# Performance work log

Measured on AMD Instinct MI355X. Metric: run time of the kernel, lower is better.

The kernel has to match this reference:

```python
import jax, jax.numpy as jnp
import numpy as np

N_HEADS = 32
N_KV_HEADS = 8
HEAD_DIM = 128
N_QUERY = N_HEADS // N_KV_HEADS  # 4
ROPE_BASE = 10000.0


def _rope_tables(seq_len, head_dim):
    # inv freqs over pairs of channels (Llama-style interleaved complex rotation)
    inv_freq = 1.0 / (ROPE_BASE ** (jnp.arange(0, head_dim, 2, dtype=jnp.float32) / head_dim))
    t = jnp.arange(seq_len, dtype=jnp.float32)
    ang = t[:, None] * inv_freq[None, :]           # [s, d/2]
    return jnp.cos(ang)[None, :, None, :], jnp.sin(ang)[None, :, None, :]  # [1,s,1,d/2]


def _apply_rope(x, cos, sin):
    # x: [b, s, h, d]; consecutive channel pairs are (real, imag)
    xr = x[..., 0::2]
    xi = x[..., 1::2]
    out_r = xr * cos - xi * sin
    out_i = xr * sin + xi * cos
    return jnp.stack([out_r, out_i], axis=-1).reshape(x.shape)


def setup_inputs() -> dict:
    key = jax.random.key(0)
    kx, kq, kk, kv, ko = jax.random.split(key, 5)
    dim = 4096
    kv_dim = N_KV_HEADS * HEAD_DIM
    scale = 0.02
    return {
        "x": jax.random.normal(kx, (2, 2048, dim), dtype=jnp.float32),
        "wq": jax.random.normal(kq, (dim, dim), dtype=jnp.float32) * scale,
        "wk": jax.random.normal(kk, (dim, kv_dim), dtype=jnp.float32) * scale,
        "wv": jax.random.normal(kv, (dim, kv_dim), dtype=jnp.float32) * scale,
        "wo": jax.random.normal(ko, (dim, dim), dtype=jnp.float32) * scale,
    }


def reference(x, wq, wk, wv, wo):
    b, s, _ = x.shape
    xq = (x @ wq).reshape(b, s, N_HEADS, HEAD_DIM)
    xk = (x @ wk).reshape(b, s, N_KV_HEADS, HEAD_DIM)
    xv = (x @ wv).reshape(b, s, N_KV_HEADS, HEAD_DIM)

    cos, sin = _rope_tables(s, HEAD_DIM)
    xq = _apply_rope(xq, cos, sin)
    xk = _apply_rope(xk, cos, sin)

    # GQA without materializing the KV expand: group query heads per kv head.
    qh = xq.reshape(b, s, N_KV_HEADS, N_QUERY, HEAD_DIM)
    scores = jnp.einsum('bsgnd,btgd->bgnst', qh, xk) / jnp.sqrt(
        jnp.asarray(HEAD_DIM, dtype=xq.dtype))  # [b,g,n,s,t]

    # causal mask: -inf above diagonal
    causal = jnp.arange(s)[:, None] >= jnp.arange(s)[None, :]
    scores = jnp.where(causal[None, None, None, :, :], scores, -jnp.inf)

    att = jax.nn.softmax(scores.astype(jnp.float32), axis=-1).astype(xq.dtype)
    out = jnp.einsum('bgnst,btgd->bsgnd', att, xv).reshape(b, s, N_HEADS * HEAD_DIM)
    return out @ wo
```

## Files before the change

### kernel.cpp

```cpp
#include <hip/hip_runtime.h>
#include <hip/hip_bf16.h>

typedef __attribute__((ext_vector_type(8))) short short8;
typedef __attribute__((ext_vector_type(4))) float f32x4;
typedef __attribute__((ext_vector_type(16))) float f32x16;

#define GLD16(gp, lp) __builtin_amdgcn_global_load_lds( \
    (const __attribute__((address_space(1))) unsigned int*)(gp), \
    (__attribute__((address_space(3))) unsigned int*)(lp), 16, 0, 0)

static __device__ __forceinline__ float bf2f(unsigned short u) {
    union { unsigned int i; float f; } v; v.i = ((unsigned int)u) << 16; return v.f;
}
static __device__ __forceinline__ short f2bf(float f) {
    union { float f; unsigned int i; } v; v.f = f;
    unsigned int r = v.i + 0x7FFFu + ((v.i >> 16) & 1u);
    return (short)(r >> 16);
}
static __device__ __forceinline__ unsigned int pack2bf(float lo, float hi) {
    return ((unsigned int)(unsigned short)f2bf(hi) << 16) | (unsigned int)(unsigned short)f2bf(lo);
}
static __device__ __forceinline__ unsigned int cvtpk(float lo, float hi) {
    unsigned int w;
    asm("v_cvt_pk_bf16_f32 %0, %1, %2" : "=v"(w) : "v"(lo), "v"(hi));
    return w;
}

__global__ void cast_f32_bf16(const float* __restrict__ src, short* __restrict__ dst, int n) {
    int i = (blockIdx.x * 256 + threadIdx.x) * 4;
    if (i >= n) return;
    float4 v = *(const float4*)(src + i);
    short4 o;
    o.x = f2bf(v.x); o.y = f2bf(v.y); o.z = f2bf(v.z); o.w = f2bf(v.w);
    *(short4*)(dst + i) = o;
}

__global__ void transpose_cast(const float* __restrict__ src, short* __restrict__ dst,
                               int N, int dstStride) {
    __shared__ float tile[32][33];
    int k0 = blockIdx.x * 32, n0 = blockIdx.y * 32;
    int t = threadIdx.x, c = t & 31, r = t >> 5;
#pragma unroll
    for (int p = 0; p < 4; ++p)
        tile[r + p * 8][c] = src[(size_t)(k0 + r + p * 8) * N + n0 + c];
    __syncthreads();
#pragma unroll
    for (int p = 0; p < 4; ++p)
        dst[(size_t)(n0 + r + p * 8) * dstStride + k0 + c] = f2bf(tile[c][r + p * 8]);
}

__global__ void transpose_v(const short* __restrict__ qkv, short* __restrict__ vt) {
    __shared__ short tile[32][33];
    int s0 = blockIdx.x * 32, d0 = blockIdx.y * 32;
    int bh = blockIdx.z;
    int b = bh >> 3, h = bh & 7;
    const short* src = qkv + (size_t)b * 2048 * 6144 + 5120 + h * 128;
    short* dst = vt + (size_t)bh * 128 * 2048;
    int t = threadIdx.x, c = t & 31, r = t >> 5;
#pragma unroll
    for (int p = 0; p < 4; ++p)
        tile[r + p * 8][c] = src[(size_t)(s0 + r + p * 8) * 6144 + d0 + c];
    __syncthreads();
#pragma unroll
    for (int p = 0; p < 4; ++p)
        dst[(size_t)(d0 + r + p * 8) * 2048 + s0 + c] = tile[c][r + p * 8];
}

__global__ void rope_tables(float* __restrict__ cs) {
    int i = blockIdx.x * 256 + threadIdx.x;
    int s = i >> 6, d2 = i & 63;
    float inv = expf(-9.210340371976184f * (float)(2 * d2) * (1.0f / 128.0f));
    float ang = (float)s * inv;
    float sn, c;
    sincosf(ang, &sn, &c);
    cs[(size_t)i * 2] = c;
    cs[(size_t)i * 2 + 1] = sn;
}

template<int NH>
__global__ void rope_apply(const short* __restrict__ qkv, const float* __restrict__ cs,
                           short* __restrict__ dst, int colOff, float scale) {
    int i = blockIdx.x * 256 + threadIdx.x;
    int d2 = i & 63;
    int t2 = i >> 6;
    int h = t2 % NH;
    int bs = t2 / NH;
    int s = bs & 2047;
    int b = bs >> 11;
    unsigned int pr = *(const unsigned int*)(qkv + (size_t)bs * 6144 + colOff + h * 128 + 2 * d2);
    float xr = bf2f((unsigned short)(pr & 0xFFFFu));
    float xi = bf2f((unsigned short)(pr >> 16));
    const float* cp = cs + ((size_t)s * 64 + d2) * 2;
    float c = cp[0], sn = cp[1];
    float outr = (xr * c - xi * sn) * scale;
    float outi = (xr * sn + xi * c) * scale;
    *(unsigned int*)(dst + ((size_t)(b * NH + h) * 2048 + s) * 128 + 2 * d2) = pack2bf(outr, outi);
}

template<bool BF16OUT>
__global__ __launch_bounds__(512, 1) void gemm256(const short* __restrict__ A,
                                                  const short* __restrict__ Bt,
                                                  void* __restrict__ Cv,
                                                  int Mtiles, int N, int K) {
    extern __shared__ __align__(16) short lds[];
    short* As = lds;
    short* Bs = lds + 32768;
    const int tid = threadIdx.x;
    const int lane = tid & 63;
    const int wid = tid >> 6;
    const int lr = lane & 15;
    const int lq = lane >> 4;
    const int wr = wid >> 2;
    const int wc = wid & 3;

    const int nwg = gridDim.x;
    const int id = blockIdx.x;
    const int sid = (id & 7) * (nwg >> 3) + (id >> 3);
    const int m0 = (sid % Mtiles) * 256;
    const int n0 = (sid / Mtiles) * 256;

    const short* aBase = A + (size_t)m0 * K;
    const short* bBase = Bt + (size_t)n0 * K;
    const int NT = K >> 5;

    auto stage = [&](int t) {
        const int buf = t & 3;
#pragma unroll
        for (int j = 0; j < 2; ++j) {
            int cl = j * 512 + tid;
            int lrw = cl >> 3;
            int cs = (cl & 7) ^ (lrw & 7);
            int trow = lrw + ((cs & 4) << 5);
            int kc = (cs & 3) * 8;
            GLD16(aBase + (size_t)trow * K + t * 32 + kc, As + buf * 8192 + cl * 8);
        }
#pragma unroll
        for (int j = 0; j < 2; ++j) {
            int cl = j * 512 + tid;
            int lrw = cl >> 3;
            int cs = (cl & 7) ^ (lrw & 7);
            int trow = lrw + ((cs & 4) << 5);
            int kc = (cs & 3) * 8;
            GLD16(bBase + (size_t)trow * K + t * 32 + kc, Bs + buf * 8192 + cl * 8);
        }
    };

    f32x4 acc[8][4];
#pragma unroll
    for (int mi = 0; mi < 8; ++mi)
#pragma unroll
        for (int ni = 0; ni < 4; ++ni) acc[mi][ni] = f32x4{0.f, 0.f, 0.f, 0.f};

    stage(0); stage(1); stage(2);
    asm volatile("s_waitcnt vmcnt(8)" ::: "memory");
    __builtin_amdgcn_sched_barrier(0);
    __builtin_amdgcn_s_barrier();
    __builtin_amdgcn_sched_barrier(0);

    for (int t = 0; t < NT; ++t) {
        const int buf = t & 3;
        if (t + 3 < NT) stage(t + 3);

        short8 af[8], bfr[4];
#pragma unroll
        for (int mi = 0; mi < 8; ++mi) {
            int lrw = (wr * 128 + mi * 16 + lr) & 127;
            int chunk = ((wr << 2) | lq) ^ (lrw & 7);
            af[mi] = *(const short8*)(As + buf * 8192 + lrw * 64 + chunk * 8);
        }
#pragma unroll
        for (int ni = 0; ni < 4; ++ni) {
            int tc = wc * 64 + ni * 16 + lr;
            int lrw = tc & 127;
            int chunk = (((tc >> 7) << 2) | lq) ^ (lrw & 7);
            bfr[ni] = *(const short8*)(Bs + buf * 8192 + lrw * 64 + chunk * 8);
        }

        __builtin_amdgcn_s_setprio(1);
#pragma unroll
        for (int mi = 0; mi < 8; ++mi)
#pragma unroll
            for (int ni = 0; ni < 4; ++ni)
                acc[mi][ni] = __builtin_amdgcn_mfma_f32_16x16x32_bf16(af[mi], bfr[ni], acc[mi][ni], 0, 0, 0);
        __builtin_amdgcn_s_setprio(0);

        __builtin_amdgcn_sched_barrier(0);
        if (t + 3 < NT)       { asm volatile("s_waitcnt vmcnt(8)" ::: "memory"); }
        else if (t + 3 == NT) { asm volatile("s_waitcnt vmcnt(4)" ::: "memory"); }
        else if (t + 2 == NT) { asm volatile("s_waitcnt vmcnt(0)" ::: "memory"); }
        __builtin_amdgcn_sched_barrier(0);
        if (t + 1 < NT) {
            __builtin_amdgcn_s_barrier();
            __builtin_amdgcn_sched_barrier(0);
        }
    }

#pragma unroll
    for (int mi = 0; mi < 8; ++mi)
#pragma unroll
        for (int ni = 0; ni < 4; ++ni)
#pragma unroll
            for (int r = 0; r < 4; ++r) {
                int row = m0 + wr * 128 + mi * 16 + lq * 4 + r;
                int col = n0 + wc * 64 + ni * 16 + lr;
                float v = acc[mi][ni][r];
                if constexpr (BF16OUT) ((short*)Cv)[(size_t)row * N + col] = f2bf(v);
                else                   ((float*)Cv)[(size_t)row * N + col] = v;
            }
}

__global__ __launch_bounds__(256, 2) void attn_kernel(const short* __restrict__ Qr,
                                                      const short* __restrict__ Kr,
                                                      const short* __restrict__ Vt,
                                                      short* __restrict__ Out) {
    __shared__ short Ks[64 * 128];
    __shared__ short Vs[128 * 64];
    const int qb = 15 - blockIdx.x;
    const int bh = blockIdx.y;
    const int b = bh >> 5;
    const int qh = bh & 31;
    const int kvh = qh >> 2;
    const int tid = threadIdx.x;
    const int lane = tid & 63;
    const int w = tid >> 6;
    const int l31 = lane & 31;
    const int hi = lane >> 5;
    const int qg0 = qb * 128 + w * 32;

    const short* qbase = Qr + ((size_t)bh * 2048 + qg0 + l31) * 128 + hi * 8;
    short8 qf[8];
#pragma unroll
    for (int ks = 0; ks < 8; ++ks)
        qf[ks] = *(const short8*)(qbase + ks * 16);

    const short* kbase = Kr + (size_t)(b * 8 + kvh) * 2048 * 128;
    const short* vbase = Vt + (size_t)(b * 8 + kvh) * 128 * 2048;

    float m_run = -INFINITY, l_run = 0.0f;
    f32x16 oacc[4];
#pragma unroll
    for (int dt = 0; dt < 4; ++dt) oacc[dt] = f32x16{0,0,0,0,0,0,0,0,0,0,0,0,0,0,0,0};

    const int nkb = 2 * qb + 2;
    for (int kb = 0; kb < nkb; ++kb) {
        const int s0 = kb * 64;
#pragma unroll
        for (int j = 0; j < 4; ++j) {
            int c = j * 256 + tid;
            int krow = c >> 4;
            int kcol = ((c & 15) ^ (krow & 7)) * 8;
            GLD16(kbase + (size_t)(s0 + krow) * 128 + kcol, Ks + (size_t)c * 8);
            int vrow = c >> 3;
            int vcol = ((c & 7) ^ (vrow & 7)) * 8;
            GLD16(vbase + (size_t)vrow * 2048 + s0 + vcol, Vs + (size_t)c * 8);
        }
        __syncthreads();

        if (s0 <= qg0 + 31) {
            f32x16 st0 = f32x16{0,0,0,0,0,0,0,0,0,0,0,0,0,0,0,0};
            f32x16 st1 = f32x16{0,0,0,0,0,0,0,0,0,0,0,0,0,0,0,0};
            __builtin_amdgcn_s_setprio(1);
#pragma unroll
            for (int ks = 0; ks < 8; ++ks) {
                int row0 = l31;
                int ch0 = ((2 * ks + hi) ^ (row0 & 7)) * 8;
                short8 kf0 = *(const short8*)(Ks + row0 * 128 + ch0);
                st0 = __builtin_amdgcn_mfma_f32_32x32x16_bf16(kf0, qf[ks], st0, 0, 0, 0);
                int row1 = 32 + l31;
                int ch1 = ((2 * ks + hi) ^ (row1 & 7)) * 8;
                short8 kf1 = *(const short8*)(Ks + row1 * 128 + ch1);
                st1 = __builtin_amdgcn_mfma_f32_32x32x16_bf16(kf1, qf[ks], st1, 0, 0, 0);
            }
            __builtin_amdgcn_s_setprio(0);

            const int q = qg0 + l31;
            if (s0 + 63 > qg0) {
#pragma unroll
                for (int i = 0; i < 16; ++i) {
                    int kvr = (i & 3) + 8 * (i >> 2) + 4 * hi;
                    if (s0 + kvr > q)      st0[i] = -INFINITY;
                    if (s0 + 32 + kvr > q) st1[i] = -INFINITY;
                }
            }

            float mx = -INFINITY;
#pragma unroll
            for (int i = 0; i < 16; ++i) mx = fmaxf(mx, fmaxf(st0[i], st1[i]));
            mx = fmaxf(mx, __shfl_xor(mx, 32, 64));

            const bool defer = __all(mx - m_run <= 8.0f);
            float mN, alpha;
            if (defer) { mN = m_run; alpha = 1.0f; }
            else       { mN = fmaxf(m_run, mx); alpha = __expf(m_run - mN); }

            float p0[16], p1[16];
            float rsum = 0.0f;
#pragma unroll
            for (int i = 0; i < 16; ++i) {
                p0[i] = __expf(st0[i] - mN);
                p1[i] = __expf(st1[i] - mN);
                rsum += p0[i] + p1[i];
            }
            rsum += __shfl_xor(rsum, 32, 64);
            l_run = l_run * alpha + rsum;
            m_run = mN;
            if (!defer) {
#pragma unroll
                for (int dt = 0; dt < 4; ++dt)
#pragma unroll
                    for (int i = 0; i < 16; ++i) oacc[dt][i] *= alpha;
            }

            short8 pfr[4];
#pragma unroll
            for (int kvs = 0; kvs < 4; ++kvs) {
                const float* pp = (kvs < 2) ? p0 : p1;
                const int h8 = (kvs & 1) * 8;
                unsigned int x0 = cvtpk(pp[h8 + 0], pp[h8 + 1]);
                unsigned int x1 = cvtpk(pp[h8 + 2], pp[h8 + 3]);
                unsigned int y0 = cvtpk(pp[h8 + 4], pp[h8 + 5]);
                unsigned int y1 = cvtpk(pp[h8 + 6], pp[h8 + 7]);
                asm("v_permlane32_swap_b32 %0, %1" : "+v"(x0), "+v"(y0));
                asm("v_permlane32_swap_b32 %0, %1" : "+v"(x1), "+v"(y1));
                union { unsigned int u[4]; short8 s; } uu;
                uu.u[0] = x0; uu.u[1] = x1; uu.u[2] = y0; uu.u[3] = y1;
                pfr[kvs] = uu.s;
            }

            __builtin_amdgcn_s_setprio(1);
#pragma unroll
            for (int dt = 0; dt < 4; ++dt) {
                int row = dt * 32 + l31;
#pragma unroll
                for (int kvs = 0; kvs < 4; ++kvs) {
                    int ch = ((2 * kvs + hi) ^ (row & 7)) * 8;
                    short8 vf = *(const short8*)(Vs + row * 64 + ch);
                    oacc[dt] = __builtin_amdgcn_mfma_f32_32x32x16_bf16(vf, pfr[kvs], oacc[dt], 0, 0, 0);
                }
            }
            __builtin_amdgcn_s_setprio(0);
        }
        __syncthreads();
    }

    const float inv = 1.0f / l_run;
    const size_t row = (size_t)b * 2048 + qg0 + l31;
    short* obase = Out + row * 4096 + qh * 128;
#pragma unroll
    for (int dt = 0; dt < 4; ++dt) {
#pragma unroll
        for (int g = 0; g < 4; ++g) {
            short4 o4;
            o4.x = f2bf(oacc[dt][g * 4 + 0] * inv);
            o4.y = f2bf(oacc[dt][g * 4 + 1] * inv);
            o4.z = f2bf(oacc[dt][g * 4 + 2] * inv);
            o4.w = f2bf(oacc[dt][g * 4 + 3] * inv);
            *(short4*)(obase + dt * 32 + g * 8 + hi * 4) = o4;
        }
    }
}


extern "C" void kernel_launch(void* const* d_in, const int* in_sizes, int n_in,
                              void* d_out, int out_size, void* d_ws, size_t ws_size,
                              hipStream_t stream) {
    const float* x  = (const float*)d_in[0];
    const float* wq = (const float*)d_in[1];
    const float* wk = (const float*)d_in[2];
    const float* wv = (const float*)d_in[3];
    const float* wo = (const float*)d_in[4];
    float* out = (float*)d_out;
    char* ws = (char*)d_ws;

    short* wt_qkv = (short*)(ws + 0);
    short* xb     = (short*)(ws + 50331648);
    short* qkv    = (short*)(ws + 83886080);
    short* wt_o   = (short*)(ws + 83886080);
    short* qr     = (short*)(ws + 134217728);
    short* kr     = (short*)(ws + 167772160);
    short* vt     = (short*)(ws + 176160768);
    float* tab    = (float*)(ws + 184549376);

    cast_f32_bf16<<<16384, 256, 0, stream>>>(x, xb, 16777216);
    transpose_cast<<<dim3(128, 128), 256, 0, stream>>>(wq, wt_qkv, 4096, 4096);
    transpose_cast<<<dim3(128, 32),  256, 0, stream>>>(wk, wt_qkv + (size_t)4096 * 4096, 1024, 4096);
    transpose_cast<<<dim3(128, 32),  256, 0, stream>>>(wv, wt_qkv + (size_t)5120 * 4096, 1024, 4096);
    rope_tables<<<512, 256, 0, stream>>>(tab);
    gemm256<true><<<384, 512, 131072, stream>>>(xb, wt_qkv, (void*)qkv, 16, 6144, 4096);
    rope_apply<32><<<32768, 256, 0, stream>>>(qkv, tab, qr, 0, 0.08838834764831845f);
    rope_apply<8><<<8192, 256, 0, stream>>>(qkv, tab, kr, 4096, 1.0f);
    transpose_v<<<dim3(64, 4, 16), 256, 0, stream>>>(qkv, vt);
    transpose_cast<<<dim3(128, 128), 256, 0, stream>>>(wo, wt_o, 4096, 4096);
    attn_kernel<<<dim3(16, 64), 256, 0, stream>>>(qr, kr, vt, xb);
    gemm256<false><<<256, 512, 131072, stream>>>(xb, wt_o, (void*)out, 16, 4096, 4096);
}
```

Measured before the change: 617.9 us.

## Split GEMM K-step into two MFMA phases with interleaved A/B staging

The bf16 GEMM main loop now runs each K-step in two halves. Each half reads its four A fragments from LDS, issues one operand's global-to-LDS prefetch (A in the first half, B in the second), and then runs a 4x4 block of MFMAs. The aim is to interleave LDS reads, global prefetches and matrix math more finely so memory latency hides behind compute. The cost is extra workgroup barriers and lgkmcnt waits per iteration, which may add sync stalls.

```diff
diff --git a/kernel.cpp b/kernel.cpp
--- a/kernel.cpp
+++ b/kernel.cpp
@@ -123,7 +123,7 @@
     const short* bBase = Bt + (size_t)n0 * K;
     const int NT = K >> 5;
 
-    auto stage = [&](int t) {
+    auto stageA = [&](int t) {
         const int buf = t & 3;
 #pragma unroll
         for (int j = 0; j < 2; ++j) {
@@ -134,6 +134,9 @@
             int kc = (cs & 3) * 8;
             GLD16(aBase + (size_t)trow * K + t * 32 + kc, As + buf * 8192 + cl * 8);
         }
+    };
+    auto stageB = [&](int t) {
+        const int buf = t & 3;
 #pragma unroll
         for (int j = 0; j < 2; ++j) {
             int cl = j * 512 + tid;
@@ -151,7 +154,7 @@
 #pragma unroll
         for (int ni = 0; ni < 4; ++ni) acc[mi][ni] = f32x4{0.f, 0.f, 0.f, 0.f};
 
-    stage(0); stage(1); stage(2);
+    stageA(0); stageB(0); stageA(1); stageB(1); stageA(2); stageB(2);
     asm volatile("s_waitcnt vmcnt(8)" ::: "memory");
     __builtin_amdgcn_sched_barrier(0);
     __builtin_amdgcn_s_barrier();
@@ -159,12 +162,11 @@
 
     for (int t = 0; t < NT; ++t) {
         const int buf = t & 3;
-        if (t + 3 < NT) stage(t + 3);
-
         short8 af[8], bfr[4];
-#pragma unroll
-        for (int mi = 0; mi < 8; ++mi) {
-            int lrw = (wr * 128 + mi * 16 + lr) & 127;
+
+#pragma unroll
+        for (int mi = 0; mi < 4; ++mi) {
+            int lrw = mi * 16 + lr;
             int chunk = ((wr << 2) | lq) ^ (lrw & 7);
             af[mi] = *(const short8*)(As + buf * 8192 + lrw * 64 + chunk * 8);
         }
@@ -175,16 +177,42 @@
             int chunk = (((tc >> 7) << 2) | lq) ^ (lrw & 7);
             bfr[ni] = *(const short8*)(Bs + buf * 8192 + lrw * 64 + chunk * 8);
         }
-
+        if (t + 3 < NT) stageA(t + 3);
+        __builtin_amdgcn_sched_barrier(0);
+        __builtin_amdgcn_s_barrier();
+        asm volatile("s_waitcnt lgkmcnt(0)" ::: "memory");
+        __builtin_amdgcn_sched_barrier(0);
         __builtin_amdgcn_s_setprio(1);
 #pragma unroll
-        for (int mi = 0; mi < 8; ++mi)
+        for (int mi = 0; mi < 4; ++mi)
 #pragma unroll
             for (int ni = 0; ni < 4; ++ni)
                 acc[mi][ni] = __builtin_amdgcn_mfma_f32_16x16x32_bf16(af[mi], bfr[ni], acc[mi][ni], 0, 0, 0);
         __builtin_amdgcn_s_setprio(0);
-
-        __builtin_amdgcn_sched_barrier(0);
+        __builtin_amdgcn_sched_barrier(0);
+        __builtin_amdgcn_s_barrier();
+        __builtin_amdgcn_sched_barrier(0);
+
+#pragma unroll
+        for (int mi = 4; mi < 8; ++mi) {
+            int lrw = mi * 16 + lr;
+            int chunk = ((wr << 2) | lq) ^ (lrw & 7);
+            af[mi] = *(const short8*)(As + buf * 8192 + lrw * 64 + chunk * 8);
+        }
+        if (t + 3 < NT) stageB(t + 3);
+        __builtin_amdgcn_sched_barrier(0);
+        __builtin_amdgcn_s_barrier();
+        asm volatile("s_waitcnt lgkmcnt(0)" ::: "memory");
+        __builtin_amdgcn_sched_barrier(0);
+        __builtin_amdgcn_s_setprio(1);
+#pragma unroll
+        for (int mi = 4; mi < 8; ++mi)
+#pragma unroll
+            for (int ni = 0; ni < 4; ++ni)
+                acc[mi][ni] = __builtin_amdgcn_mfma_f32_16x16x32_bf16(af[mi], bfr[ni], acc[mi][ni], 0, 0, 0);
+        __builtin_amdgcn_s_setprio(0);
+        __builtin_amdgcn_sched_barrier(0);
+
         if (t + 3 < NT)       { asm volatile("s_waitcnt vmcnt(8)" ::: "memory"); }
         else if (t + 3 == NT) { asm volatile("s_waitcnt vmcnt(4)" ::: "memory"); }
         else if (t + 2 == NT) { asm volatile("s_waitcnt vmcnt(0)" ::: "memory"); }
```

Result: no change. 623.8 us (+1.0%).

## Replace QKV projection GEMM with smaller 128x128-tile kernel

Applied to the files above, without the earlier changes.

Adds a new GEMM kernel using 128x128 output tiles, 256 threads, static LDS and two blocks per CU, and uses it for the QKV projection instead of the 256-tile kernel with 131 KB of dynamic LDS. The aim is more blocks for better occupancy and load balance across CUs (1536 blocks vs 384). In exchange it loses the larger tile's data reuse and any pipelining the old kernel had, since the new loop is single-buffered with a sync before and after compute. It also writes bf16 outputs one element at a time, uncoalesced.

```diff
diff --git a/kernel.cpp b/kernel.cpp
--- a/kernel.cpp
+++ b/kernel.cpp
@@ -98,6 +98,81 @@
 }
 
 template<bool BF16OUT>
+__global__ __launch_bounds__(256, 2) void gemm_bt(const short* __restrict__ A,
+                                                  const short* __restrict__ Bt,
+                                                  void* __restrict__ Cv,
+                                                  int Mtiles, int N, int K) {
+    __shared__ short As[128 * 64];
+    __shared__ short Bs[128 * 64];
+    const int tid = threadIdx.x;
+    const int lane = tid & 63;
+    const int wid = tid >> 6;
+    const int lr = lane & 15;
+    const int lq = lane >> 4;
+    const int nwg = gridDim.x;
+    const int id = blockIdx.x;
+    const int sid = (id & 7) * (nwg >> 3) + (id >> 3);
+    const int m0 = (sid % Mtiles) * 128;
+    const int n0 = (sid / Mtiles) * 128;
+    const int wr = (wid >> 1) * 64;
+    const int wc = (wid & 1) * 64;
+    f32x4 acc[4][4];
+#pragma unroll
+    for (int i = 0; i < 4; ++i)
+#pragma unroll
+        for (int j = 0; j < 4; ++j) acc[i][j] = f32x4{0.f, 0.f, 0.f, 0.f};
+
+    const short* aBase = A + (size_t)m0 * K;
+    const short* bBase = Bt + (size_t)n0 * K;
+
+    for (int k0 = 0; k0 < K; k0 += 64) {
+#pragma unroll
+        for (int j = 0; j < 4; ++j) {
+            int c = (wid * 4 + j) * 64 + lane;
+            int row = c >> 3;
+            int cb = ((c & 7) << 4) ^ ((row & 7) << 4);
+            GLD16(aBase + (size_t)row * K + k0 + (cb >> 1), As + (wid * 4 + j) * 512);
+            GLD16(bBase + (size_t)row * K + k0 + (cb >> 1), Bs + (wid * 4 + j) * 512);
+        }
+        __syncthreads();
+#pragma unroll
+        for (int ks = 0; ks < 2; ++ks) {
+            short8 af[4], bfr[4];
+#pragma unroll
+            for (int mi = 0; mi < 4; ++mi) {
+                int row = wr + mi * 16 + lr;
+                int cb = (ks * 64 + lq * 16) ^ ((row & 7) << 4);
+                af[mi] = *(const short8*)(As + row * 64 + (cb >> 1));
+            }
+#pragma unroll
+            for (int ni = 0; ni < 4; ++ni) {
+                int row = wc + ni * 16 + lr;
+                int cb = (ks * 64 + lq * 16) ^ ((row & 7) << 4);
+                bfr[ni] = *(const short8*)(Bs + row * 64 + (cb >> 1));
+            }
+#pragma unroll
+            for (int mi = 0; mi < 4; ++mi)
+#pragma unroll
+                for (int ni = 0; ni < 4; ++ni)
+                    acc[mi][ni] = __builtin_amdgcn_mfma_f32_16x16x32_bf16(af[mi], bfr[ni], acc[mi][ni], 0, 0, 0);
+        }
+        __syncthreads();
+    }
+#pragma unroll
+    for (int mi = 0; mi < 4; ++mi)
+#pragma unroll
+        for (int ni = 0; ni < 4; ++ni)
+#pragma unroll
+            for (int r = 0; r < 4; ++r) {
+                int row = m0 + wr + mi * 16 + lq * 4 + r;
+                int col = n0 + wc + ni * 16 + lr;
+                float v = acc[mi][ni][r];
+                if constexpr (BF16OUT) ((short*)Cv)[(size_t)row * N + col] = f2bf(v);
+                else                   ((float*)Cv)[(size_t)row * N + col] = v;
+            }
+}
+
+template<bool BF16OUT>
 __global__ __launch_bounds__(512, 1) void gemm256(const short* __restrict__ A,
                                                   const short* __restrict__ Bt,
                                                   void* __restrict__ Cv,
@@ -386,7 +461,7 @@
     transpose_cast<<<dim3(128, 32),  256, 0, stream>>>(wk, wt_qkv + (size_t)4096 * 4096, 1024, 4096);
     transpose_cast<<<dim3(128, 32),  256, 0, stream>>>(wv, wt_qkv + (size_t)5120 * 4096, 1024, 4096);
     rope_tables<<<512, 256, 0, stream>>>(tab);
-    gemm256<true><<<384, 512, 131072, stream>>>(xb, wt_qkv, (void*)qkv, 16, 6144, 4096);
+    gemm_bt<true><<<1536, 256, 0, stream>>>(xb, wt_qkv, (void*)qkv, 32, 6144, 4096);
     rope_apply<32><<<32768, 256, 0, stream>>>(qkv, tab, qr, 0, 0.08838834764831845f);
     rope_apply<8><<<8192, 256, 0, stream>>>(qkv, tab, kr, 4096, 1.0f);
     transpose_v<<<dim3(64, 4, 16), 256, 0, stream>>>(qkv, vt);
```

Measured after the change: 621.8 us. About the same (+0.6%).
